# Kernel optimization log

Hardware: AMD Instinct MI355X
Metric: run time of the kernel (lower is better)

The kernel has to match this reference:

```python
import jax, jax.numpy as jnp
import numpy as np

D_MODEL = 512
MEM_DIM = 64
DECAY_LOGIT_INIT = 2.9444389791664403  # logit(0.95)


def setup_inputs() -> dict:
    key = jax.random.key(0)
    ks = jax.random.split(key, 6)
    B, L = 2, 2048
    x = jax.random.normal(ks[0], (B, L, D_MODEL), dtype=jnp.float32)
    s = 1.0 / np.sqrt(D_MODEL)
    W_q = jax.random.normal(ks[1], (MEM_DIM, D_MODEL), dtype=jnp.float32) * s
    W_k = jax.random.normal(ks[2], (MEM_DIM, D_MODEL), dtype=jnp.float32) * s
    W_v = jax.random.normal(ks[3], (D_MODEL, D_MODEL), dtype=jnp.float32) * s
    W_o = jax.random.normal(ks[4], (D_MODEL, D_MODEL), dtype=jnp.float32) * s
    decay_logit = jnp.asarray(DECAY_LOGIT_INIT, dtype=jnp.float32)
    norm_w = jnp.ones((D_MODEL,), dtype=jnp.float32)
    return {"x": x, "W_q": W_q, "W_k": W_k, "W_v": W_v, "W_o": W_o,
            "decay_logit": decay_logit, "norm_w": norm_w}


def _rms_norm(x, w, eps=1e-6):
    dtype = x.dtype
    x_f = x.astype(jnp.float32)
    rms = jnp.sqrt(jnp.mean(x_f * x_f, axis=-1, keepdims=True) + eps)
    return (x_f / rms).astype(dtype) * w.astype(dtype)


def reference(x, W_q, W_k, W_v, W_o, decay_logit, norm_w):
    B, L, D = x.shape
    M = W_q.shape[0]
    scale = M ** (-0.5)
    phi = lambda t: jax.nn.elu(t) + 1.0  # positive kernel
    queries = phi(x @ W_q.T) * scale          # (B,L,M)
    keys = phi(x @ W_k.T)                     # (B,L,M)
    values = x @ W_v.T                        # (B,L,D)

    decay = jax.nn.sigmoid(decay_logit)
    log_decay = jnp.log(jnp.clip(decay, 1e-6))
    positions = jnp.arange(L, dtype=x.dtype)
    log_cum = jnp.clip(log_decay * positions, -20.0, 20.0)  # (L,)
    exp_neg = jnp.exp(-log_cum)[None, :, None]              # (1,L,1)
    exp_pos = jnp.exp(log_cum)[None, :, None]

    # fast-weight write: M_t = exp_pos_t * cumsum_s<=t exp_neg_s * k_s^T v_s
    kv = keys[..., :, None] * values[..., None, :]          # (B,L,M,D)
    cum_kv = jnp.cumsum(exp_neg[..., None] * kv, axis=1)
    Mem = exp_pos[..., None] * cum_kv                       # (B,L,M,D)

    z = exp_pos * jnp.cumsum(exp_neg * keys, axis=1)        # (B,L,M)

    numerator = jnp.einsum('blm,blmd->bld', queries, Mem)
    denominator = jnp.einsum('blm,blm->bl', queries, z)[..., None] + 1e-6
    out = _rms_norm(numerator / denominator, norm_w)
    return out @ W_o.T
```

## Files before the change

kernel.cpp:

```cpp
#include <hip/hip_runtime.h>
#include <math.h>

#define NB 2
#define LSEQ 2048
#define DM 512
#define MM 64
#define CHK 64
#define NCHUNK 32

typedef __attribute__((ext_vector_type(8))) short short8v;
typedef __attribute__((ext_vector_type(4))) float f32x4;

__device__ __forceinline__ float get_ld(const float* __restrict__ logit) {
    float lg = *logit;
    float dec = 1.0f / (1.0f + expf(-lg));
    dec = fmaxf(dec, 1e-6f);
    return logf(dec);
}
__device__ __forceinline__ float cpos(float ld, int t) {
    return fminf(fmaxf(ld * (float)t, -20.0f), 20.0f);
}
__device__ __forceinline__ float phi_fn(float v) {
    return v > 0.0f ? v + 1.0f : expf(v);
}
__device__ __forceinline__ unsigned short f2bf(float f) {
    unsigned int u = __float_as_uint(f);
    u += 0x7FFFu + ((u >> 16) & 1u);
    return (unsigned short)(u >> 16);
}
__device__ __forceinline__ float bf2f(unsigned short h) {
    unsigned int u = ((unsigned int)h) << 16;
    return __uint_as_float(u);
}
__device__ __forceinline__ uint4 cvt8(const float* __restrict__ p) {
    float4 a = *(const float4*)p;
    float4 b = *(const float4*)(p + 4);
    union { unsigned short u[8]; uint4 v; } r;
    r.u[0] = f2bf(a.x); r.u[1] = f2bf(a.y); r.u[2] = f2bf(a.z); r.u[3] = f2bf(a.w);
    r.u[4] = f2bf(b.x); r.u[5] = f2bf(b.y); r.u[6] = f2bf(b.z); r.u[7] = f2bf(b.w);
    return r.v;
}

__global__ __launch_bounds__(256) void gemm_proj(
    const float* __restrict__ x, const float* __restrict__ W_q,
    const float* __restrict__ W_k, const float* __restrict__ W_v,
    const float* __restrict__ W_o,
    unsigned short* __restrict__ Qh, unsigned short* __restrict__ Kh,
    unsigned short* __restrict__ Vh, unsigned short* __restrict__ Wob)
{
    const int cb = blockIdx.y;
    const int tid = threadIdx.x;
    if (cb == 5) {
        const int stride = 64 * 256;
#pragma unroll
        for (int it = 0; it < 4; ++it) {
            int i = blockIdx.x * 256 + tid + it * stride;
            float4 v = ((const float4*)W_o)[i];
            ushort4 o;
            o.x = f2bf(v.x); o.y = f2bf(v.y); o.z = f2bf(v.z); o.w = f2bf(v.w);
            ((ushort4*)Wob)[i] = o;
        }
        return;
    }

    __shared__ unsigned short As[64][40];
    __shared__ unsigned short Bs[128][40];
    const int brow = blockIdx.x * 64;
    const int lane = tid & 63, wid = tid >> 6;
    const int wr = wid >> 1, wc = wid & 1;
    const int lr = lane & 15, lk = lane >> 4;

    f32x4 acc[2][4];
#pragma unroll
    for (int i = 0; i < 2; ++i)
#pragma unroll
        for (int j = 0; j < 4; ++j) acc[i][j] = (f32x4)(0.f);

    for (int k0 = 0; k0 < DM; k0 += 32) {
        {
            const int r = tid >> 2, kg = tid & 3;
            *(uint4*)&As[r][kg * 8] = cvt8(&x[(size_t)(brow + r) * DM + k0 + kg * 8]);
        }
#pragma unroll
        for (int i = 0; i < 2; ++i) {
            int c = tid * 2 + i;
            int r = c >> 2, kg = c & 3;
            const float* wsrc;
            if (cb == 0)
                wsrc = (r < 64) ? &W_q[(size_t)r * DM + k0 + kg * 8]
                                : &W_k[(size_t)(r - 64) * DM + k0 + kg * 8];
            else
                wsrc = &W_v[(size_t)((cb - 1) * 128 + r) * DM + k0 + kg * 8];
            *(uint4*)&Bs[r][kg * 8] = cvt8(wsrc);
        }
        __syncthreads();
        short8v af[2], bf[4];
#pragma unroll
        for (int mt = 0; mt < 2; ++mt)
            af[mt] = *(const short8v*)&As[wr * 32 + mt * 16 + lr][lk * 8];
#pragma unroll
        for (int nt = 0; nt < 4; ++nt)
            bf[nt] = *(const short8v*)&Bs[wc * 64 + nt * 16 + lr][lk * 8];
#pragma unroll
        for (int mt = 0; mt < 2; ++mt)
#pragma unroll
            for (int nt = 0; nt < 4; ++nt)
                acc[mt][nt] = __builtin_amdgcn_mfma_f32_16x16x32_bf16(
                    af[mt], bf[nt], acc[mt][nt], 0, 0, 0);
        __syncthreads();
    }

#pragma unroll
    for (int mt = 0; mt < 2; ++mt)
#pragma unroll
        for (int nt = 0; nt < 4; ++nt) {
            const int col = wc * 64 + nt * 16 + lr;
#pragma unroll
            for (int j = 0; j < 4; ++j) {
                const int row = brow + wr * 32 + mt * 16 + lk * 4 + j;
                float v = acc[mt][nt][j];
                if (cb == 0) {
                    v = phi_fn(v);
                    if (col < 64)
                        Qh[(size_t)row * MM + col] = f2bf(v * 0.125f);
                    else
                        Kh[(size_t)row * MM + (col - 64)] = f2bf(v);
                } else {
                    Vh[(size_t)row * DM + (cb - 1) * 128 + col] = f2bf(v);
                }
            }
        }
}

__global__ __launch_bounds__(256) void chunk_local_mfma(
    const unsigned short* __restrict__ Qb, const unsigned short* __restrict__ Kb,
    const unsigned short* __restrict__ Vb, const float* __restrict__ logit,
    unsigned short* __restrict__ OI, float* __restrict__ DI,
    unsigned short* __restrict__ KV, float* __restrict__ KZ)
{
    const int chunk = blockIdx.x, dg = blockIdx.y, b = blockIdx.z;
    const int tid = threadIdx.x;
    const int lane = tid & 63, wid = tid >> 6;
    const int wr = wid >> 1, wc = wid & 1;
    const int lr = lane & 15, lk = lane >> 4;
    const int t0 = chunk * CHK;
    const float ld = get_ld(logit);

    __shared__ unsigned short Qs[64][72];
    __shared__ unsigned short Ks[64][72];
    __shared__ unsigned short As[64][72];
    __shared__ unsigned short Kws[64][66];
    __shared__ unsigned short Vs[64][134];
    __shared__ float wks[64];
    __shared__ float cps[64];
    __shared__ float DIsh[64];

    if (tid < 64) {
        const float c = cpos(ld, t0 + tid);
        cps[tid] = c;
        wks[tid] = expf(cpos(ld, t0 + CHK - 1) - c);
        DIsh[tid] = 0.f;
    }
    __syncthreads();

    const unsigned short* Qg = Qb + ((size_t)b * LSEQ + t0) * MM;
    const unsigned short* Kg = Kb + ((size_t)b * LSEQ + t0) * MM;
#pragma unroll
    for (int l = 0; l < 2; ++l) {
        const int e = tid + l * 256;
        const int r = e >> 3, gq = e & 7;
        *(uint4*)&Qs[r][gq * 8] = *(const uint4*)(Qg + (size_t)e * 8);
        uint4 kraw = *(const uint4*)(Kg + (size_t)e * 8);
        *(uint4*)&Ks[r][gq * 8] = kraw;
        const float w = wks[r];
        const unsigned short* kp = (const unsigned short*)&kraw;
#pragma unroll
        for (int p = 0; p < 4; ++p) {
            ushort2 o;
            o.x = f2bf(w * bf2f(kp[2 * p]));
            o.y = f2bf(w * bf2f(kp[2 * p + 1]));
            *(ushort2*)&Kws[r][gq * 8 + 2 * p] = o;
        }
    }
    const unsigned short* Vg = Vb + ((size_t)b * LSEQ + t0) * DM + dg * 128;
#pragma unroll
    for (int l = 0; l < 4; ++l) {
        const int e = tid + l * 256;
        const int s = e >> 4, gg = e & 15;
        uint4 vr = *(const uint4*)(Vg + (size_t)s * DM + gg * 8);
        const unsigned short* vp = (const unsigned short*)&vr;
#pragma unroll
        for (int p = 0; p < 4; ++p) {
            ushort2 o;
            o.x = vp[2 * p]; o.y = vp[2 * p + 1];
            *(ushort2*)&Vs[s][gg * 8 + 2 * p] = o;
        }
    }
    __syncthreads();

    f32x4 sacc[2][2];
#pragma unroll
    for (int i = 0; i < 2; ++i)
#pragma unroll
        for (int j = 0; j < 2; ++j) sacc[i][j] = (f32x4)(0.f);
#pragma unroll
    for (int ks = 0; ks < 2; ++ks) {
        short8v qa[2], kb2[2];
#pragma unroll
        for (int mt = 0; mt < 2; ++mt)
            qa[mt] = *(const short8v*)&Qs[wr * 32 + mt * 16 + lr][ks * 32 + lk * 8];
#pragma unroll
        for (int nt = 0; nt < 2; ++nt)
            kb2[nt] = *(const short8v*)&Ks[wc * 32 + nt * 16 + lr][ks * 32 + lk * 8];
#pragma unroll
        for (int mt = 0; mt < 2; ++mt)
#pragma unroll
            for (int nt = 0; nt < 2; ++nt)
                sacc[mt][nt] = __builtin_amdgcn_mfma_f32_16x16x32_bf16(
                    qa[mt], kb2[nt], sacc[mt][nt], 0, 0, 0);
    }

#pragma unroll
    for (int mt = 0; mt < 2; ++mt) {
#pragma unroll
        for (int j = 0; j < 4; ++j) {
            const int t = wr * 32 + mt * 16 + lk * 4 + j;
            const float ct = cps[t];
            float rowpart = 0.f;
#pragma unroll
            for (int nt = 0; nt < 2; ++nt) {
                const int s = wc * 32 + nt * 16 + lr;
                float v = sacc[mt][nt][j];
                v = (s <= t) ? v * expf(ct - cps[s]) : 0.f;
                rowpart += v;
                As[t][s] = f2bf(v);
            }
            rowpart += __shfl_xor(rowpart, 1);
            rowpart += __shfl_xor(rowpart, 2);
            rowpart += __shfl_xor(rowpart, 4);
            rowpart += __shfl_xor(rowpart, 8);
            if (lr == 0) atomicAdd(&DIsh[t], rowpart);
        }
    }
    __syncthreads();

    if (dg == 0) {
        if (tid < 64) DI[(size_t)b * LSEQ + t0 + tid] = DIsh[tid];
        if (tid >= 64 && tid < 128) {
            const int m = tid - 64;
            float z = 0.f;
#pragma unroll
            for (int s = 0; s < 64; ++s) z += wks[s] * bf2f(Ks[s][m]);
            KZ[((size_t)b * NCHUNK + chunk) * MM + m] = z;
        }
    }

    f32x4 aO[2][4], aK[2][4];
#pragma unroll
    for (int i = 0; i < 2; ++i)
#pragma unroll
        for (int j = 0; j < 4; ++j) { aO[i][j] = (f32x4)(0.f); aK[i][j] = (f32x4)(0.f); }

#pragma unroll
    for (int ks = 0; ks < 2; ++ks) {
        short8v vf[4];
#pragma unroll
        for (int nt = 0; nt < 4; ++nt) {
            unsigned short* vp = (unsigned short*)&vf[nt];
            const int n = wc * 64 + nt * 16 + lr;
#pragma unroll
            for (int e = 0; e < 8; ++e)
                vp[e] = Vs[ks * 32 + lk * 8 + e][n];
        }
        short8v af2[2], kf2[2];
#pragma unroll
        for (int mt = 0; mt < 2; ++mt) {
            const int row = wr * 32 + mt * 16 + lr;
            af2[mt] = *(const short8v*)&As[row][ks * 32 + lk * 8];
            unsigned short* kp = (unsigned short*)&kf2[mt];
#pragma unroll
            for (int e = 0; e < 8; ++e)
                kp[e] = Kws[ks * 32 + lk * 8 + e][row];
        }
#pragma unroll
        for (int mt = 0; mt < 2; ++mt)
#pragma unroll
            for (int nt = 0; nt < 4; ++nt) {
                aO[mt][nt] = __builtin_amdgcn_mfma_f32_16x16x32_bf16(
                    af2[mt], vf[nt], aO[mt][nt], 0, 0, 0);
                aK[mt][nt] = __builtin_amdgcn_mfma_f32_16x16x32_bf16(
                    kf2[mt], vf[nt], aK[mt][nt], 0, 0, 0);
            }
    }

    unsigned short* OIb = OI + ((size_t)b * LSEQ + t0) * DM + dg * 128;
    unsigned short* KVb = KV + ((size_t)b * NCHUNK + chunk) * MM * DM + dg * 128;
#pragma unroll
    for (int mt = 0; mt < 2; ++mt)
#pragma unroll
        for (int nt = 0; nt < 4; ++nt) {
            const int col = wc * 64 + nt * 16 + lr;
#pragma unroll
            for (int j = 0; j < 4; ++j) {
                const int row = wr * 32 + mt * 16 + lk * 4 + j;
                OIb[(size_t)row * DM + col] = f2bf(aO[mt][nt][j]);
                KVb[(size_t)row * DM + col] = f2bf(aK[mt][nt][j]);
            }
        }
}

__global__ __launch_bounds__(128) void state_scan(
    const unsigned short* __restrict__ KV, const float* __restrict__ KZ,
    const float* __restrict__ logit,
    unsigned short* __restrict__ SS, float* __restrict__ ZS)
{
    const int g = blockIdx.x * 128 + threadIdx.x;
    const int b = g >> 15;
    const int rem = g & 32767;
    const int m = rem >> 9;
    const int d = rem & 511;
    const float ld = get_ld(logit);
    const size_t base = (((size_t)b * NCHUNK) * MM + m) * DM + d;
    const size_t cstride = (size_t)MM * DM;

    float v[NCHUNK];
#pragma unroll
    for (int i = 0; i < NCHUNK; ++i) v[i] = bf2f(KV[base + (size_t)i * cstride]);

    float s = 0.f, cprev = 0.f;
#pragma unroll
    for (int i = 0; i < NCHUNK; ++i) {
        const float ce = cpos(ld, i * CHK + CHK - 1);
        const float lam = expf(ce - cprev);
        cprev = ce;
        SS[base + (size_t)i * cstride] = f2bf(s);
        s = lam * s + v[i];
    }
    if (d == 0) {
        float zs = 0.f;
        cprev = 0.f;
#pragma unroll
        for (int i = 0; i < NCHUNK; ++i) {
            const float ce = cpos(ld, i * CHK + CHK - 1);
            const float lam = expf(ce - cprev);
            cprev = ce;
            const int zi = (b * NCHUNK + i) * MM + m;
            ZS[zi] = zs;
            zs = lam * zs + KZ[zi];
        }
    }
}

__global__ __launch_bounds__(256) void combine_rms(
    const unsigned short* __restrict__ Qb, const unsigned short* __restrict__ SSb,
    const float* __restrict__ ZS, const unsigned short* __restrict__ OI,
    const float* __restrict__ DI, const float* __restrict__ logit,
    const float* __restrict__ norm_w, unsigned short* __restrict__ NRM)
{
    const int chunk = blockIdx.x, quarter = blockIdx.y, b = blockIdx.z;
    const int tid = threadIdx.x;
    const int lane = tid & 63, w = tid >> 6;
    const int lr = lane & 15, lk = lane >> 4;
    const int t0 = chunk * CHK;
    const int r0 = quarter * 16;
    const float ld = get_ld(logit);

    __shared__ unsigned short Qs[16][72];
    __shared__ unsigned short Ssh[64][514];
    __shared__ float wsh[512];
    __shared__ float gv[16], invden[16], xsq[16], rinv[16];

    if (tid < 128) {
        const unsigned short* Qg = Qb + ((size_t)b * LSEQ + t0 + r0) * MM;
        const int r = tid >> 3, g8 = tid & 7;
        *(uint4*)&Qs[r][g8 * 8] = *(const uint4*)(Qg + (size_t)tid * 8);
    }
    {
        const unsigned short* Sg = SSb + ((size_t)(b * NCHUNK + chunk) * MM) * DM;
#pragma unroll
        for (int l = 0; l < 16; ++l) {
            const int e = tid + l * 256;
            const int m = e >> 6, g8 = e & 63;
            uint4 v = *(const uint4*)(Sg + (size_t)m * DM + g8 * 8);
            const unsigned short* vp = (const unsigned short*)&v;
#pragma unroll
            for (int p = 0; p < 4; ++p) {
                ushort2 o; o.x = vp[2 * p]; o.y = vp[2 * p + 1];
                *(ushort2*)&Ssh[m][g8 * 8 + 2 * p] = o;
            }
        }
    }
    wsh[tid] = norm_w[tid];
    wsh[tid + 256] = norm_w[tid + 256];
    if (tid < 16) {
        const float cprev = (chunk > 0) ? cpos(ld, t0 - 1) : 0.f;
        gv[tid] = expf(cpos(ld, t0 + r0 + tid) - cprev);
        xsq[tid] = 0.f;
    }
    __syncthreads();

    if (tid < 16) {
        const float* zp = ZS + ((size_t)b * NCHUNK + chunk) * MM;
        float a = 0.f;
#pragma unroll
        for (int m = 0; m < MM; ++m) a += bf2f(Qs[tid][m]) * zp[m];
        invden[tid] = 1.0f /
            (gv[tid] * a + DI[(size_t)b * LSEQ + t0 + r0 + tid] + 1e-6f);
    }

    f32x4 acc[8];
#pragma unroll
    for (int j = 0; j < 8; ++j) acc[j] = (f32x4)(0.f);

#pragma unroll
    for (int ks = 0; ks < 2; ++ks) {
        short8v vf[8];
#pragma unroll
        for (int nt = 0; nt < 8; ++nt) {
            unsigned short* vp = (unsigned short*)&vf[nt];
            const int col = w * 128 + nt * 16 + lr;
#pragma unroll
            for (int e = 0; e < 8; ++e)
                vp[e] = Ssh[ks * 32 + lk * 8 + e][col];
        }
        short8v af = *(const short8v*)&Qs[lr][ks * 32 + lk * 8];
#pragma unroll
        for (int nt = 0; nt < 8; ++nt)
            acc[nt] = __builtin_amdgcn_mfma_f32_16x16x32_bf16(
                af, vf[nt], acc[nt], 0, 0, 0);
    }
    __syncthreads();

    const unsigned short* OIb = OI + ((size_t)b * LSEQ + t0 + r0) * DM;
#pragma unroll
    for (int j = 0; j < 4; ++j) {
        const int row = lk * 4 + j;
        const float g = gv[row];
        const float inv = invden[row];
        float part = 0.f;
#pragma unroll
        for (int nt = 0; nt < 8; ++nt) {
            const int col = w * 128 + nt * 16 + lr;
            float v = g * acc[nt][j] + bf2f(OIb[(size_t)row * DM + col]);
            float xx = v * inv;
            acc[nt][j] = xx;
            part += xx * xx;
        }
        part += __shfl_xor(part, 1);
        part += __shfl_xor(part, 2);
        part += __shfl_xor(part, 4);
        part += __shfl_xor(part, 8);
        if (lr == 0) atomicAdd(&xsq[row], part);
    }
    __syncthreads();
    if (tid < 16)
        rinv[tid] = 1.0f / sqrtf(xsq[tid] * (1.0f / (float)DM) + 1e-6f);
    __syncthreads();

    unsigned short* NRMc = NRM + ((size_t)b * LSEQ + t0 + r0) * DM;
#pragma unroll
    for (int j = 0; j < 4; ++j) {
        const int row = lk * 4 + j;
        const float r = rinv[row];
#pragma unroll
        for (int nt = 0; nt < 8; ++nt) {
            const int col = w * 128 + nt * 16 + lr;
            NRMc[(size_t)row * DM + col] = f2bf(acc[nt][j] * r * wsh[col]);
        }
    }
}

__global__ __launch_bounds__(256) void gemm_out(
    const unsigned short* __restrict__ Xb, const unsigned short* __restrict__ Wb,
    float* __restrict__ C)
{
    __shared__ unsigned short As[64][40];
    __shared__ unsigned short Bs[128][40];
    const int brow = blockIdx.x * 64;
    const int bcol = blockIdx.y * 128;
    const int tid = threadIdx.x;
    const int lane = tid & 63, wid = tid >> 6;
    const int wr = wid >> 1, wc = wid & 1;
    const int lr = lane & 15, lk = lane >> 4;

    f32x4 acc[2][4];
#pragma unroll
    for (int i = 0; i < 2; ++i)
#pragma unroll
        for (int j = 0; j < 4; ++j) acc[i][j] = (f32x4)(0.f);

    for (int k0 = 0; k0 < DM; k0 += 32) {
        {
            const int r = tid >> 2, kg = tid & 3;
            *(uint4*)&As[r][kg * 8] =
                *(const uint4*)&Xb[(size_t)(brow + r) * DM + k0 + kg * 8];
        }
#pragma unroll
        for (int i = 0; i < 2; ++i) {
            int c = tid * 2 + i;
            int r = c >> 2, kg = c & 3;
            *(uint4*)&Bs[r][kg * 8] =
                *(const uint4*)&Wb[(size_t)(bcol + r) * DM + k0 + kg * 8];
        }
        __syncthreads();
        short8v af[2], bf[4];
#pragma unroll
        for (int mt = 0; mt < 2; ++mt)
            af[mt] = *(const short8v*)&As[wr * 32 + mt * 16 + lr][lk * 8];
#pragma unroll
        for (int nt = 0; nt < 4; ++nt)
            bf[nt] = *(const short8v*)&Bs[wc * 64 + nt * 16 + lr][lk * 8];
#pragma unroll
        for (int mt = 0; mt < 2; ++mt)
#pragma unroll
            for (int nt = 0; nt < 4; ++nt)
                acc[mt][nt] = __builtin_amdgcn_mfma_f32_16x16x32_bf16(
                    af[mt], bf[nt], acc[mt][nt], 0, 0, 0);
        __syncthreads();
    }

#pragma unroll
    for (int mt = 0; mt < 2; ++mt)
#pragma unroll
        for (int nt = 0; nt < 4; ++nt) {
            const int row0 = brow + wr * 32 + mt * 16 + lk * 4;
            const int col = bcol + wc * 64 + nt * 16 + lr;
#pragma unroll
            for (int j = 0; j < 4; ++j)
                C[(size_t)(row0 + j) * DM + col] = acc[mt][nt][j];
        }
}

extern "C" void kernel_launch(void* const* d_in, const int* in_sizes, int n_in,
                              void* d_out, int out_size, void* d_ws, size_t ws_size,
                              hipStream_t stream) {
    const float* x      = (const float*)d_in[0];
    const float* W_q    = (const float*)d_in[1];
    const float* W_k    = (const float*)d_in[2];
    const float* W_v    = (const float*)d_in[3];
    const float* W_o    = (const float*)d_in[4];
    const float* logit  = (const float*)d_in[5];
    const float* norm_w = (const float*)d_in[6];
    float* out = (float*)d_out;

    const size_t BLM = (size_t)NB * LSEQ * MM;
    const size_t BLD = (size_t)NB * LSEQ * DM;
    const size_t BL  = (size_t)NB * LSEQ;
    const size_t BNCMD = (size_t)NB * NCHUNK * MM * DM;
    const size_t BNCM  = (size_t)NB * NCHUNK * MM;
    const size_t WSZ = (size_t)DM * DM;

    float* ws = (float*)d_ws;
    float* DIp = ws;
    float* KZp = DIp + BL;
    float* ZSp = KZp + BNCM;
    unsigned short* OIb  = (unsigned short*)(ZSp + BNCM);
    unsigned short* KVb  = OIb + BLD;
    unsigned short* SSb  = KVb + BNCMD;
    unsigned short* Wob16 = SSb + BNCMD;
    unsigned short* Qb16 = Wob16 + WSZ;
    unsigned short* Kb16 = Qb16 + BLM;
    unsigned short* Vb16 = Kb16 + BLM;
    unsigned short* NRMb = Vb16 + BLD;

    gemm_proj<<<dim3(64, 6), 256, 0, stream>>>(x, W_q, W_k, W_v, W_o,
                                               Qb16, Kb16, Vb16, Wob16);
    chunk_local_mfma<<<dim3(NCHUNK, 4, NB), 256, 0, stream>>>(
        Qb16, Kb16, Vb16, logit, OIb, DIp, KVb, KZp);
    state_scan<<<dim3(512), 128, 0, stream>>>(KVb, KZp, logit, SSb, ZSp);
    combine_rms<<<dim3(NCHUNK, 4, NB), 256, 0, stream>>>(
        Qb16, SSb, ZSp, OIb, DIp, logit, norm_w, NRMb);
    gemm_out<<<dim3(64, 4), 256, 0, stream>>>(NRMb, Wob16, out);
}
```

Before: 61.84 us.

## Double block size to 512 threads and redistribute per-wave MFMA work

Four kernels now launch 512-thread blocks (8 waves) instead of 256 with the same grid. Each wave handles half as many output tiles, which cuts accumulator registers and spreads the load and MFMA work. In chunk_local_mfma the intra-chunk output and the chunk KV-state products go to separate wave groups instead of being computed together by every wave. The aim is more latency hiding and memory parallelism per block in these small, launch-bound kernels. The cost is that each B fragment is reused across fewer tiles, so shared-memory traffic per MFMA rises, and some load phases leave half the threads idle.

```diff
diff --git a/kernel.cpp b/kernel.cpp
--- a/kernel.cpp
+++ b/kernel.cpp
@@ -41,7 +41,7 @@
     return r.v;
 }
 
-__global__ __launch_bounds__(256) void gemm_proj(
+__global__ __launch_bounds__(512) void gemm_proj(
     const float* __restrict__ x, const float* __restrict__ W_q,
     const float* __restrict__ W_k, const float* __restrict__ W_v,
     const float* __restrict__ W_o,
@@ -51,10 +51,10 @@
     const int cb = blockIdx.y;
     const int tid = threadIdx.x;
     if (cb == 5) {
-        const int stride = 64 * 256;
-#pragma unroll
-        for (int it = 0; it < 4; ++it) {
-            int i = blockIdx.x * 256 + tid + it * stride;
+        const int stride = 64 * 512;
+#pragma unroll
+        for (int it = 0; it < 2; ++it) {
+            int i = blockIdx.x * 512 + tid + it * stride;
             float4 v = ((const float4*)W_o)[i];
             ushort4 o;
             o.x = f2bf(v.x); o.y = f2bf(v.y); o.z = f2bf(v.z); o.w = f2bf(v.w);
@@ -66,25 +66,23 @@
     __shared__ unsigned short As[64][40];
     __shared__ unsigned short Bs[128][40];
     const int brow = blockIdx.x * 64;
-    const int lane = tid & 63, wid = tid >> 6;
-    const int wr = wid >> 1, wc = wid & 1;
+    const int lane = tid & 63, w = tid >> 6;
+    const int wr = w >> 2, wc = w & 3;
     const int lr = lane & 15, lk = lane >> 4;
 
-    f32x4 acc[2][4];
+    f32x4 acc[2][2];
 #pragma unroll
     for (int i = 0; i < 2; ++i)
 #pragma unroll
-        for (int j = 0; j < 4; ++j) acc[i][j] = (f32x4)(0.f);
+        for (int j = 0; j < 2; ++j) acc[i][j] = (f32x4)(0.f);
 
     for (int k0 = 0; k0 < DM; k0 += 32) {
+        if (tid < 256) {
+            const int r = tid >> 2, kg = tid & 3;
+            *(uint4*)&As[r][kg * 8] = cvt8(&x[(size_t)(brow + r) * DM + k0 + kg * 8]);
+        }
         {
             const int r = tid >> 2, kg = tid & 3;
-            *(uint4*)&As[r][kg * 8] = cvt8(&x[(size_t)(brow + r) * DM + k0 + kg * 8]);
-        }
-#pragma unroll
-        for (int i = 0; i < 2; ++i) {
-            int c = tid * 2 + i;
-            int r = c >> 2, kg = c & 3;
             const float* wsrc;
             if (cb == 0)
                 wsrc = (r < 64) ? &W_q[(size_t)r * DM + k0 + kg * 8]
@@ -94,17 +92,17 @@
             *(uint4*)&Bs[r][kg * 8] = cvt8(wsrc);
         }
         __syncthreads();
-        short8v af[2], bf[4];
+        short8v af[2], bf[2];
 #pragma unroll
         for (int mt = 0; mt < 2; ++mt)
             af[mt] = *(const short8v*)&As[wr * 32 + mt * 16 + lr][lk * 8];
 #pragma unroll
-        for (int nt = 0; nt < 4; ++nt)
-            bf[nt] = *(const short8v*)&Bs[wc * 64 + nt * 16 + lr][lk * 8];
+        for (int nt = 0; nt < 2; ++nt)
+            bf[nt] = *(const short8v*)&Bs[wc * 32 + nt * 16 + lr][lk * 8];
 #pragma unroll
         for (int mt = 0; mt < 2; ++mt)
 #pragma unroll
-            for (int nt = 0; nt < 4; ++nt)
+            for (int nt = 0; nt < 2; ++nt)
                 acc[mt][nt] = __builtin_amdgcn_mfma_f32_16x16x32_bf16(
                     af[mt], bf[nt], acc[mt][nt], 0, 0, 0);
         __syncthreads();
@@ -113,8 +111,8 @@
 #pragma unroll
     for (int mt = 0; mt < 2; ++mt)
 #pragma unroll
-        for (int nt = 0; nt < 4; ++nt) {
-            const int col = wc * 64 + nt * 16 + lr;
+        for (int nt = 0; nt < 2; ++nt) {
+            const int col = wc * 32 + nt * 16 + lr;
 #pragma unroll
             for (int j = 0; j < 4; ++j) {
                 const int row = brow + wr * 32 + mt * 16 + lk * 4 + j;
@@ -132,7 +130,7 @@
         }
 }
 
-__global__ __launch_bounds__(256) void chunk_local_mfma(
+__global__ __launch_bounds__(512) void chunk_local_mfma(
     const unsigned short* __restrict__ Qb, const unsigned short* __restrict__ Kb,
     const unsigned short* __restrict__ Vb, const float* __restrict__ logit,
     unsigned short* __restrict__ OI, float* __restrict__ DI,
@@ -140,8 +138,7 @@
 {
     const int chunk = blockIdx.x, dg = blockIdx.y, b = blockIdx.z;
     const int tid = threadIdx.x;
-    const int lane = tid & 63, wid = tid >> 6;
-    const int wr = wid >> 1, wc = wid & 1;
+    const int lane = tid & 63, w = tid >> 6;
     const int lr = lane & 15, lk = lane >> 4;
     const int t0 = chunk * CHK;
     const float ld = get_ld(logit);
@@ -163,74 +160,66 @@
     }
     __syncthreads();
 
-    const unsigned short* Qg = Qb + ((size_t)b * LSEQ + t0) * MM;
-    const unsigned short* Kg = Kb + ((size_t)b * LSEQ + t0) * MM;
-#pragma unroll
-    for (int l = 0; l < 2; ++l) {
-        const int e = tid + l * 256;
-        const int r = e >> 3, gq = e & 7;
-        *(uint4*)&Qs[r][gq * 8] = *(const uint4*)(Qg + (size_t)e * 8);
-        uint4 kraw = *(const uint4*)(Kg + (size_t)e * 8);
+    {
+        const unsigned short* Qg = Qb + ((size_t)b * LSEQ + t0) * MM;
+        const unsigned short* Kg = Kb + ((size_t)b * LSEQ + t0) * MM;
+        const int r = tid >> 3, gq = tid & 7;
+        *(uint4*)&Qs[r][gq * 8] = *(const uint4*)(Qg + (size_t)tid * 8);
+        uint4 kraw = *(const uint4*)(Kg + (size_t)tid * 8);
         *(uint4*)&Ks[r][gq * 8] = kraw;
-        const float w = wks[r];
+        const float wv = wks[r];
         const unsigned short* kp = (const unsigned short*)&kraw;
 #pragma unroll
         for (int p = 0; p < 4; ++p) {
             ushort2 o;
-            o.x = f2bf(w * bf2f(kp[2 * p]));
-            o.y = f2bf(w * bf2f(kp[2 * p + 1]));
+            o.x = f2bf(wv * bf2f(kp[2 * p]));
+            o.y = f2bf(wv * bf2f(kp[2 * p + 1]));
             *(ushort2*)&Kws[r][gq * 8 + 2 * p] = o;
         }
     }
-    const unsigned short* Vg = Vb + ((size_t)b * LSEQ + t0) * DM + dg * 128;
-#pragma unroll
-    for (int l = 0; l < 4; ++l) {
-        const int e = tid + l * 256;
-        const int s = e >> 4, gg = e & 15;
-        uint4 vr = *(const uint4*)(Vg + (size_t)s * DM + gg * 8);
-        const unsigned short* vp = (const unsigned short*)&vr;
-#pragma unroll
-        for (int p = 0; p < 4; ++p) {
-            ushort2 o;
-            o.x = vp[2 * p]; o.y = vp[2 * p + 1];
-            *(ushort2*)&Vs[s][gg * 8 + 2 * p] = o;
-        }
-    }
-    __syncthreads();
-
-    f32x4 sacc[2][2];
-#pragma unroll
-    for (int i = 0; i < 2; ++i)
-#pragma unroll
-        for (int j = 0; j < 2; ++j) sacc[i][j] = (f32x4)(0.f);
-#pragma unroll
-    for (int ks = 0; ks < 2; ++ks) {
-        short8v qa[2], kb2[2];
-#pragma unroll
-        for (int mt = 0; mt < 2; ++mt)
-            qa[mt] = *(const short8v*)&Qs[wr * 32 + mt * 16 + lr][ks * 32 + lk * 8];
-#pragma unroll
-        for (int nt = 0; nt < 2; ++nt)
-            kb2[nt] = *(const short8v*)&Ks[wc * 32 + nt * 16 + lr][ks * 32 + lk * 8];
-#pragma unroll
-        for (int mt = 0; mt < 2; ++mt)
+    {
+        const unsigned short* Vg = Vb + ((size_t)b * LSEQ + t0) * DM + dg * 128;
+#pragma unroll
+        for (int l = 0; l < 2; ++l) {
+            const int e = tid + l * 512;
+            const int s = e >> 4, gg = e & 15;
+            uint4 vr = *(const uint4*)(Vg + (size_t)s * DM + gg * 8);
+            const unsigned short* vp = (const unsigned short*)&vr;
+#pragma unroll
+            for (int p = 0; p < 4; ++p) {
+                ushort2 o;
+                o.x = vp[2 * p]; o.y = vp[2 * p + 1];
+                *(ushort2*)&Vs[s][gg * 8 + 2 * p] = o;
+            }
+        }
+    }
+    __syncthreads();
+
+    {
+        const int wr2 = w >> 1, wc2 = w & 1;
+        f32x4 sacc[2];
+        sacc[0] = (f32x4)(0.f); sacc[1] = (f32x4)(0.f);
+#pragma unroll
+        for (int ks = 0; ks < 2; ++ks) {
+            short8v qa = *(const short8v*)&Qs[wr2 * 16 + lr][ks * 32 + lk * 8];
+            short8v kb2[2];
 #pragma unroll
             for (int nt = 0; nt < 2; ++nt)
-                sacc[mt][nt] = __builtin_amdgcn_mfma_f32_16x16x32_bf16(
-                    qa[mt], kb2[nt], sacc[mt][nt], 0, 0, 0);
-    }
-
-#pragma unroll
-    for (int mt = 0; mt < 2; ++mt) {
+                kb2[nt] = *(const short8v*)&Ks[wc2 * 32 + nt * 16 + lr][ks * 32 + lk * 8];
+#pragma unroll
+            for (int nt = 0; nt < 2; ++nt)
+                sacc[nt] = __builtin_amdgcn_mfma_f32_16x16x32_bf16(
+                    qa, kb2[nt], sacc[nt], 0, 0, 0);
+        }
 #pragma unroll
         for (int j = 0; j < 4; ++j) {
-            const int t = wr * 32 + mt * 16 + lk * 4 + j;
+            const int t = wr2 * 16 + lk * 4 + j;
             const float ct = cps[t];
             float rowpart = 0.f;
 #pragma unroll
             for (int nt = 0; nt < 2; ++nt) {
-                const int s = wc * 32 + nt * 16 + lr;
-                float v = sacc[mt][nt][j];
+                const int s = wc2 * 32 + nt * 16 + lr;
+                float v = sacc[nt][j];
                 v = (s <= t) ? v * expf(ct - cps[s]) : 0.f;
                 rowpart += v;
                 As[t][s] = f2bf(v);
@@ -255,58 +244,77 @@
         }
     }
 
-    f32x4 aO[2][4], aK[2][4];
-#pragma unroll
-    for (int i = 0; i < 2; ++i)
-#pragma unroll
-        for (int j = 0; j < 4; ++j) { aO[i][j] = (f32x4)(0.f); aK[i][j] = (f32x4)(0.f); }
-
-#pragma unroll
-    for (int ks = 0; ks < 2; ++ks) {
-        short8v vf[4];
-#pragma unroll
-        for (int nt = 0; nt < 4; ++nt) {
-            unsigned short* vp = (unsigned short*)&vf[nt];
-            const int n = wc * 64 + nt * 16 + lr;
-#pragma unroll
-            for (int e = 0; e < 8; ++e)
-                vp[e] = Vs[ks * 32 + lk * 8 + e][n];
-        }
-        short8v af2[2], kf2[2];
-#pragma unroll
-        for (int mt = 0; mt < 2; ++mt) {
-            const int row = wr * 32 + mt * 16 + lr;
-            af2[mt] = *(const short8v*)&As[row][ks * 32 + lk * 8];
-            unsigned short* kp = (unsigned short*)&kf2[mt];
-#pragma unroll
-            for (int e = 0; e < 8; ++e)
-                kp[e] = Kws[ks * 32 + lk * 8 + e][row];
-        }
-#pragma unroll
-        for (int mt = 0; mt < 2; ++mt)
+    {
+        const int isKV = w >> 2;
+        const int w2 = w & 3;
+        const int wr = w2 >> 1, wc = w2 & 1;
+
+        f32x4 a2[2][4];
+#pragma unroll
+        for (int i = 0; i < 2; ++i)
+#pragma unroll
+            for (int j = 0; j < 4; ++j) a2[i][j] = (f32x4)(0.f);
+
+#pragma unroll
+        for (int ks = 0; ks < 2; ++ks) {
+            short8v vf[4];
 #pragma unroll
             for (int nt = 0; nt < 4; ++nt) {
-                aO[mt][nt] = __builtin_amdgcn_mfma_f32_16x16x32_bf16(
-                    af2[mt], vf[nt], aO[mt][nt], 0, 0, 0);
-                aK[mt][nt] = __builtin_amdgcn_mfma_f32_16x16x32_bf16(
-                    kf2[mt], vf[nt], aK[mt][nt], 0, 0, 0);
+                unsigned short* vp = (unsigned short*)&vf[nt];
+                const int n = wc * 64 + nt * 16 + lr;
+#pragma unroll
+                for (int e = 0; e < 8; ++e)
+                    vp[e] = Vs[ks * 32 + lk * 8 + e][n];
             }
-    }
-
-    unsigned short* OIb = OI + ((size_t)b * LSEQ + t0) * DM + dg * 128;
-    unsigned short* KVb = KV + ((size_t)b * NCHUNK + chunk) * MM * DM + dg * 128;
-#pragma unroll
-    for (int mt = 0; mt < 2; ++mt)
-#pragma unroll
-        for (int nt = 0; nt < 4; ++nt) {
-            const int col = wc * 64 + nt * 16 + lr;
-#pragma unroll
-            for (int j = 0; j < 4; ++j) {
-                const int row = wr * 32 + mt * 16 + lk * 4 + j;
-                OIb[(size_t)row * DM + col] = f2bf(aO[mt][nt][j]);
-                KVb[(size_t)row * DM + col] = f2bf(aK[mt][nt][j]);
+            short8v mf[2];
+#pragma unroll
+            for (int mt = 0; mt < 2; ++mt) {
+                const int row = wr * 32 + mt * 16 + lr;
+                if (!isKV) {
+                    mf[mt] = *(const short8v*)&As[row][ks * 32 + lk * 8];
+                } else {
+                    unsigned short* kp = (unsigned short*)&mf[mt];
+#pragma unroll
+                    for (int e = 0; e < 8; ++e)
+                        kp[e] = Kws[ks * 32 + lk * 8 + e][row];
+                }
             }
-        }
+#pragma unroll
+            for (int mt = 0; mt < 2; ++mt)
+#pragma unroll
+                for (int nt = 0; nt < 4; ++nt)
+                    a2[mt][nt] = __builtin_amdgcn_mfma_f32_16x16x32_bf16(
+                        mf[mt], vf[nt], a2[mt][nt], 0, 0, 0);
+        }
+
+        if (!isKV) {
+            unsigned short* OIb = OI + ((size_t)b * LSEQ + t0) * DM + dg * 128;
+#pragma unroll
+            for (int mt = 0; mt < 2; ++mt)
+#pragma unroll
+                for (int nt = 0; nt < 4; ++nt) {
+                    const int col = wc * 64 + nt * 16 + lr;
+#pragma unroll
+                    for (int j = 0; j < 4; ++j) {
+                        const int row = wr * 32 + mt * 16 + lk * 4 + j;
+                        OIb[(size_t)row * DM + col] = f2bf(a2[mt][nt][j]);
+                    }
+                }
+        } else {
+            unsigned short* KVb = KV + ((size_t)b * NCHUNK + chunk) * MM * DM + dg * 128;
+#pragma unroll
+            for (int mt = 0; mt < 2; ++mt)
+#pragma unroll
+                for (int nt = 0; nt < 4; ++nt) {
+                    const int col = wc * 64 + nt * 16 + lr;
+#pragma unroll
+                    for (int j = 0; j < 4; ++j) {
+                        const int row = wr * 32 + mt * 16 + lk * 4 + j;
+                        KVb[(size_t)row * DM + col] = f2bf(a2[mt][nt][j]);
+                    }
+                }
+        }
+    }
 }
 
 __global__ __launch_bounds__(128) void state_scan(
@@ -351,7 +359,7 @@
     }
 }
 
-__global__ __launch_bounds__(256) void combine_rms(
+__global__ __launch_bounds__(512) void combine_rms(
     const unsigned short* __restrict__ Qb, const unsigned short* __restrict__ SSb,
     const float* __restrict__ ZS, const unsigned short* __restrict__ OI,
     const float* __restrict__ DI, const float* __restrict__ logit,
@@ -378,8 +386,8 @@
     {
         const unsigned short* Sg = SSb + ((size_t)(b * NCHUNK + chunk) * MM) * DM;
 #pragma unroll
-        for (int l = 0; l < 16; ++l) {
-            const int e = tid + l * 256;
+        for (int l = 0; l < 8; ++l) {
+            const int e = tid + l * 512;
             const int m = e >> 6, g8 = e & 63;
             uint4 v = *(const uint4*)(Sg + (size_t)m * DM + g8 * 8);
             const unsigned short* vp = (const unsigned short*)&v;
@@ -391,7 +399,6 @@
         }
     }
     wsh[tid] = norm_w[tid];
-    wsh[tid + 256] = norm_w[tid + 256];
     if (tid < 16) {
         const float cprev = (chunk > 0) ? cpos(ld, t0 - 1) : 0.f;
         gv[tid] = expf(cpos(ld, t0 + r0 + tid) - cprev);
@@ -408,24 +415,24 @@
             (gv[tid] * a + DI[(size_t)b * LSEQ + t0 + r0 + tid] + 1e-6f);
     }
 
-    f32x4 acc[8];
-#pragma unroll
-    for (int j = 0; j < 8; ++j) acc[j] = (f32x4)(0.f);
+    f32x4 acc[4];
+#pragma unroll
+    for (int j = 0; j < 4; ++j) acc[j] = (f32x4)(0.f);
 
 #pragma unroll
     for (int ks = 0; ks < 2; ++ks) {
-        short8v vf[8];
-#pragma unroll
-        for (int nt = 0; nt < 8; ++nt) {
+        short8v vf[4];
+#pragma unroll
+        for (int nt = 0; nt < 4; ++nt) {
             unsigned short* vp = (unsigned short*)&vf[nt];
-            const int col = w * 128 + nt * 16 + lr;
+            const int col = w * 64 + nt * 16 + lr;
 #pragma unroll
             for (int e = 0; e < 8; ++e)
                 vp[e] = Ssh[ks * 32 + lk * 8 + e][col];
         }
         short8v af = *(const short8v*)&Qs[lr][ks * 32 + lk * 8];
 #pragma unroll
-        for (int nt = 0; nt < 8; ++nt)
+        for (int nt = 0; nt < 4; ++nt)
             acc[nt] = __builtin_amdgcn_mfma_f32_16x16x32_bf16(
                 af, vf[nt], acc[nt], 0, 0, 0);
     }
@@ -439,8 +446,8 @@
         const float inv = invden[row];
         float part = 0.f;
 #pragma unroll
-        for (int nt = 0; nt < 8; ++nt) {
-            const int col = w * 128 + nt * 16 + lr;
+        for (int nt = 0; nt < 4; ++nt) {
+            const int col = w * 64 + nt * 16 + lr;
             float v = g * acc[nt][j] + bf2f(OIb[(size_t)row * DM + col]);
             float xx = v * inv;
             acc[nt][j] = xx;
@@ -463,14 +470,14 @@
         const int row = lk * 4 + j;
         const float r = rinv[row];
 #pragma unroll
-        for (int nt = 0; nt < 8; ++nt) {
-            const int col = w * 128 + nt * 16 + lr;
+        for (int nt = 0; nt < 4; ++nt) {
+            const int col = w * 64 + nt * 16 + lr;
             NRMc[(size_t)row * DM + col] = f2bf(acc[nt][j] * r * wsh[col]);
         }
     }
 }
 
-__global__ __launch_bounds__(256) void gemm_out(
+__global__ __launch_bounds__(512) void gemm_out(
     const unsigned short* __restrict__ Xb, const unsigned short* __restrict__ Wb,
     float* __restrict__ C)
 {
@@ -479,41 +486,39 @@
     const int brow = blockIdx.x * 64;
     const int bcol = blockIdx.y * 128;
     const int tid = threadIdx.x;
-    const int lane = tid & 63, wid = tid >> 6;
-    const int wr = wid >> 1, wc = wid & 1;
+    const int lane = tid & 63, w = tid >> 6;
+    const int wr = w >> 2, wc = w & 3;
     const int lr = lane & 15, lk = lane >> 4;
 
-    f32x4 acc[2][4];
+    f32x4 acc[2][2];
 #pragma unroll
     for (int i = 0; i < 2; ++i)
 #pragma unroll
-        for (int j = 0; j < 4; ++j) acc[i][j] = (f32x4)(0.f);
+        for (int j = 0; j < 2; ++j) acc[i][j] = (f32x4)(0.f);
 
     for (int k0 = 0; k0 < DM; k0 += 32) {
-        {
+        if (tid < 256) {
             const int r = tid >> 2, kg = tid & 3;
             *(uint4*)&As[r][kg * 8] =
                 *(const uint4*)&Xb[(size_t)(brow + r) * DM + k0 + kg * 8];
         }
-#pragma unroll
-        for (int i = 0; i < 2; ++i) {
-            int c = tid * 2 + i;
-            int r = c >> 2, kg = c & 3;
+        {
+            const int r = tid >> 2, kg = tid & 3;
             *(uint4*)&Bs[r][kg * 8] =
                 *(const uint4*)&Wb[(size_t)(bcol + r) * DM + k0 + kg * 8];
         }
         __syncthreads();
-        short8v af[2], bf[4];
+        short8v af[2], bf[2];
 #pragma unroll
         for (int mt = 0; mt < 2; ++mt)
             af[mt] = *(const short8v*)&As[wr * 32 + mt * 16 + lr][lk * 8];
 #pragma unroll
-        for (int nt = 0; nt < 4; ++nt)
-            bf[nt] = *(const short8v*)&Bs[wc * 64 + nt * 16 + lr][lk * 8];
+        for (int nt = 0; nt < 2; ++nt)
+            bf[nt] = *(const short8v*)&Bs[wc * 32 + nt * 16 + lr][lk * 8];
 #pragma unroll
         for (int mt = 0; mt < 2; ++mt)
 #pragma unroll
-            for (int nt = 0; nt < 4; ++nt)
+            for (int nt = 0; nt < 2; ++nt)
                 acc[mt][nt] = __builtin_amdgcn_mfma_f32_16x16x32_bf16(
                     af[mt], bf[nt], acc[mt][nt], 0, 0, 0);
         __syncthreads();
@@ -522,9 +527,9 @@
 #pragma unroll
     for (int mt = 0; mt < 2; ++mt)
 #pragma unroll
-        for (int nt = 0; nt < 4; ++nt) {
+        for (int nt = 0; nt < 2; ++nt) {
             const int row0 = brow + wr * 32 + mt * 16 + lk * 4;
-            const int col = bcol + wc * 64 + nt * 16 + lr;
+            const int col = bcol + wc * 32 + nt * 16 + lr;
 #pragma unroll
             for (int j = 0; j < 4; ++j)
                 C[(size_t)(row0 + j) * DM + col] = acc[mt][nt][j];
@@ -563,12 +568,12 @@
     unsigned short* Vb16 = Kb16 + BLM;
     unsigned short* NRMb = Vb16 + BLD;
 
-    gemm_proj<<<dim3(64, 6), 256, 0, stream>>>(x, W_q, W_k, W_v, W_o,
+    gemm_proj<<<dim3(64, 6), 512, 0, stream>>>(x, W_q, W_k, W_v, W_o,
                                                Qb16, Kb16, Vb16, Wob16);
-    chunk_local_mfma<<<dim3(NCHUNK, 4, NB), 256, 0, stream>>>(
+    chunk_local_mfma<<<dim3(NCHUNK, 4, NB), 512, 0, stream>>>(
         Qb16, Kb16, Vb16, logit, OIb, DIp, KVb, KZp);
     state_scan<<<dim3(512), 128, 0, stream>>>(KVb, KZp, logit, SSb, ZSp);
-    combine_rms<<<dim3(NCHUNK, 4, NB), 256, 0, stream>>>(
+    combine_rms<<<dim3(NCHUNK, 4, NB), 512, 0, stream>>>(
         Qb16, SSb, ZSp, OIb, DIp, logit, norm_w, NRMb);
-    gemm_out<<<dim3(64, 4), 256, 0, stream>>>(NRMb, Wob16, out);
-}
+    gemm_out<<<dim3(64, 4), 512, 0, stream>>>(NRMb, Wob16, out);
+}
```

Measured after the change: 57.07 us. 1.08x faster.
